# Performance work log

Hardware: AMD Instinct MI355X
Metric: run time of the kernel (lower is better)

Reference implementation:

```python
import jax, jax.numpy as jnp
import numpy as np

EMBED = 1024
HEADS = 16
HEAD_DIM = EMBED // HEADS


def setup_inputs() -> dict:
    key = jax.random.key(0)
    ks = jax.random.split(key, 8)
    b, t, d = 2, 2048, EMBED
    s = 1.0 / np.sqrt(d)
    return {
        'k': jax.random.normal(ks[0], (b, t, d), jnp.float32),
        'q': jax.random.normal(ks[1], (b, t, d), jnp.float32),
        'v': jax.random.normal(ks[2], (b, t, d), jnp.float32),
        'Wk': jax.random.normal(ks[3], (d, d), jnp.float32) * s,
        'Wq': jax.random.normal(ks[4], (d, d), jnp.float32) * s,
        'Wv': jax.random.normal(ks[5], (d, d), jnp.float32) * s,
        'Wo': jax.random.normal(ks[6], (d, d), jnp.float32) * s,
        'bo': jax.random.normal(ks[7], (d,), jnp.float32) * 0.01,
    }


def reference(k, q, v, Wk, Wq, Wv, Wo, bo):
    b, t, d = q.shape
    h, n = HEADS, HEAD_DIM
    # projections (q_prj bias=False, k/v bias=False per add_bias_kv=False)
    keys = (k @ Wk.T).reshape(b, t, h, n).transpose(0, 2, 1, 3)      # b h t n
    queries = (q @ Wq.T).reshape(b, t, h, n).transpose(0, 2, 1, 3)
    values = (v @ Wv.T).reshape(b, t, h, n).transpose(0, 2, 1, 3)
    att = jnp.einsum('bhtn,bhsn->bhts', queries, keys)               # b h t t
    att = jax.nn.softmax(att / np.sqrt(n), axis=-1)
    out = jnp.einsum('bhts,bhsn->bhtn', att, values)                 # b h t n
    out = out.transpose(0, 2, 1, 3).reshape(b, t, d)                 # b t (h n)
    return out @ Wo.T + bo
```

## Files before the change

### kernel.cpp

```cpp
#include <hip/hip_runtime.h>
#include <hip/hip_bf16.h>


typedef unsigned short u16;
typedef unsigned int   u32;
using short8 = __attribute__((ext_vector_type(8))) short;
using f32x4  = __attribute__((ext_vector_type(4))) float;

__device__ __forceinline__ u16 f2b(float f) {
    u32 u = __float_as_uint(f);
    u += 0x7FFFu + ((u >> 16) & 1u);
    return (u16)(u >> 16);
}
__device__ __forceinline__ u32 pack2(float lo, float hi) {
    union { __hip_bfloat162 h; u32 u; } c;
    c.h = __float22bfloat162_rn(make_float2(lo, hi));
    return c.u;
}
__device__ __forceinline__ float fexp2(float x) {
    return __builtin_amdgcn_exp2f(x);
}
__device__ __forceinline__ void gld_lds16(const u16* g, u16* l) {
    __builtin_amdgcn_global_load_lds(
        (const __attribute__((address_space(1))) void*)g,
        (__attribute__((address_space(3))) void*)l, 16, 0, 0);
}

__global__ __launch_bounds__(256) void convert_kernel(
    const float* s0, const float* s1, const float* s2, const float* s3,
    const float* s4, const float* s5, const float* s6,
    u16* d0, u16* d1, u16* d2, u16* d3, u16* d4, u16* d5, u16* d6)
{
    const int y = blockIdx.y;
    const float* s; u16* d; u32 n;
    switch (y) {
        case 0: s = s0; d = d0; n = 1048576; break;
        case 1: s = s1; d = d1; n = 1048576; break;
        case 2: s = s2; d = d2; n = 1048576; break;
        case 3: s = s3; d = d3; n = 262144; break;
        case 4: s = s4; d = d4; n = 262144; break;
        case 5: s = s5; d = d5; n = 262144; break;
        default: s = s6; d = d6; n = 262144; break;
    }
    for (u32 i = blockIdx.x * 256 + threadIdx.x; i < n; i += 256 * 1024) {
        float4 f = ((const float4*)s)[i];
        uint2 o; o.x = pack2(f.x, f.y); o.y = pack2(f.z, f.w);
        ((uint2*)d)[i] = o;
    }
}

template <int MODE>
__device__ __forceinline__ void gemm_core(
    const u16* __restrict__ A, const u16* __restrict__ B,
    void* __restrict__ C, const float* __restrict__ bias, float scale,
    u32 bm, u32 bn)
{
    constexpr u32 K = 1024;
    __shared__ u16 As[128 * 32];
    __shared__ u16 Bs[128 * 32];

    const int tid  = threadIdx.x;
    const int lane = tid & 63;
    const int w    = tid >> 6;
    const int wr   = w >> 1, wc = w & 1;
    const int ml   = lane & 15, g = lane >> 4;

    f32x4 acc[4][4] = {};

    const u32 srow = w * 32 + (lane >> 2);
    const u32 scol = (u32)(((lane & 3) ^ ((lane >> 3) & 3)) * 8);
    const u16* gA = A + (size_t)(bm + srow) * K + scol;
    const u16* gB = B + (size_t)(bn + srow) * K + scol;
    u16* lA = &As[w * 1024];
    u16* lB = &Bs[w * 1024];

    const u32 fsw = (u32)((g ^ ((ml >> 1) & 3)) * 8);

    for (u32 k0 = 0; k0 < K; k0 += 32) {
        __syncthreads();
        gld_lds16(gA + k0, lA);
        gld_lds16(gA + 16 * K + k0, lA + 512);
        gld_lds16(gB + k0, lB);
        gld_lds16(gB + 16 * K + k0, lB + 512);
        __syncthreads();

        short8 af[4], bf[4];
#pragma unroll
        for (int it = 0; it < 4; ++it)
            af[it] = *(const short8*)&As[(wr * 64 + it * 16 + ml) * 32 + fsw];
#pragma unroll
        for (int ct = 0; ct < 4; ++ct)
            bf[ct] = *(const short8*)&Bs[(wc * 64 + ct * 16 + ml) * 32 + fsw];
#pragma unroll
        for (int it = 0; it < 4; ++it)
#pragma unroll
            for (int ct = 0; ct < 4; ++ct)
                acc[it][ct] = __builtin_amdgcn_mfma_f32_16x16x32_bf16(
                    af[it], bf[ct], acc[it][ct], 0, 0, 0);
    }

    if (MODE == 3) {
#pragma unroll
        for (int ct = 0; ct < 4; ++ct) {
            const u32 col = bn + wc * 64 + ct * 16 + ml;
            u16* dst = (u16*)C + (col >> 11) * 2097152 + (col & 2047);
#pragma unroll
            for (int it = 0; it < 4; ++it) {
                const u32 row = bm + wr * 64 + it * 16 + g * 4;
#pragma unroll
                for (int r = 0; r < 4; ++r)
                    dst[(size_t)(row + r) * 2048] = f2b(acc[it][ct][r]);
            }
        }
    } else {
#pragma unroll
        for (int ct = 0; ct < 4; ++ct) {
            const u32 col = bn + wc * 64 + ct * 16 + ml;
            const float bv = (MODE == 2 && bias) ? bias[col] : 0.0f;
#pragma unroll
            for (int it = 0; it < 4; ++it) {
                const u32 row = bm + wr * 64 + it * 16 + g * 4;
#pragma unroll
                for (int r = 0; r < 4; ++r) {
                    const float v = acc[it][ct][r] * scale + bv;
                    if (MODE == 2) ((float*)C)[(size_t)(row + r) * 1024 + col] = v;
                    else           ((u16*)C)[(size_t)(row + r) * 1024 + col] = f2b(v);
                }
            }
        }
    }
}

__global__ __launch_bounds__(256) void proj3_kernel(
    const u16* kb, const u16* qb, const u16* vb,
    const u16* Wkb, const u16* Wqb, const u16* Wvb,
    u16* Kp, u16* Qp, u16* Vt)
{
    if (blockIdx.z == 0)
        gemm_core<0>(kb, Wkb, Kp, nullptr, 1.0f, blockIdx.y * 128, blockIdx.x * 128);
    else if (blockIdx.z == 1)
        gemm_core<0>(qb, Wqb, Qp, nullptr, 0.18033688011112042f, blockIdx.y * 128, blockIdx.x * 128);
    else
        gemm_core<3>(Wvb, vb, Vt, nullptr, 1.0f, blockIdx.x * 128, blockIdx.y * 128);
}

__global__ __launch_bounds__(256) void out_gemm_kernel(
    const u16* __restrict__ A, const u16* __restrict__ W,
    float* __restrict__ C, const float* __restrict__ bias)
{
    constexpr u32 K = 1024;
    __shared__ u16 As[64 * 32];
    __shared__ u16 Bs[128 * 32];

    const int tid  = threadIdx.x;
    const int lane = tid & 63;
    const int w    = tid >> 6;
    const int wr   = w >> 1, wc = w & 1;
    const int ml   = lane & 15, g = lane >> 4;
    const u32 bm   = blockIdx.y * 64, bn = blockIdx.x * 128;

    f32x4 acc[2][4] = {};

    const u32 scol = (u32)(((lane & 3) ^ ((lane >> 3) & 3)) * 8);
    const u16* gA = A + (size_t)(bm + w * 16 + (lane >> 2)) * K + scol;
    const u16* gB = W + (size_t)(bn + w * 32 + (lane >> 2)) * K + scol;
    u16* lA = &As[w * 512];
    u16* lB = &Bs[w * 1024];

    const u32 fsw = (u32)((g ^ ((ml >> 1) & 3)) * 8);

    for (u32 k0 = 0; k0 < K; k0 += 32) {
        __syncthreads();
        gld_lds16(gA + k0, lA);
        gld_lds16(gB + k0, lB);
        gld_lds16(gB + 16 * K + k0, lB + 512);
        __syncthreads();

        short8 af[2], bf[4];
#pragma unroll
        for (int it = 0; it < 2; ++it)
            af[it] = *(const short8*)&As[(wr * 32 + it * 16 + ml) * 32 + fsw];
#pragma unroll
        for (int ct = 0; ct < 4; ++ct)
            bf[ct] = *(const short8*)&Bs[(wc * 64 + ct * 16 + ml) * 32 + fsw];
#pragma unroll
        for (int it = 0; it < 2; ++it)
#pragma unroll
            for (int ct = 0; ct < 4; ++ct)
                acc[it][ct] = __builtin_amdgcn_mfma_f32_16x16x32_bf16(
                    af[it], bf[ct], acc[it][ct], 0, 0, 0);
    }

#pragma unroll
    for (int ct = 0; ct < 4; ++ct) {
        const u32 col = bn + wc * 64 + ct * 16 + ml;
        const float bv = bias ? bias[col] : 0.0f;
#pragma unroll
        for (int it = 0; it < 2; ++it) {
            const u32 row = bm + wr * 32 + it * 16 + g * 4;
#pragma unroll
            for (int r = 0; r < 4; ++r)
                C[(size_t)(row + r) * 1024 + col] = acc[it][ct][r] + bv;
        }
    }
}

__global__ __launch_bounds__(256, 2) void attn_kernel(
    const u16* __restrict__ Qp, const u16* __restrict__ Kp,
    const u16* __restrict__ Vt, u16* __restrict__ Op)
{
    __shared__ u16   Ps[4 * 2048];
    __shared__ float R0[4096];
    __shared__ float Lr[256];

    const int tid  = threadIdx.x;
    const int lane = tid & 63;
    const int w    = tid >> 6;
    const int ml   = lane & 15;
    const int g    = lane >> 4;
    const u32 bh   = blockIdx.y;
    const u32 b    = bh >> 4, h = bh & 15;
    const u32 t0   = blockIdx.x * 64;

    const u32 base  = b * 2048 * 1024 + h * 64;
    const u32 vbase = bh * 64 * 2048;

    short8 bq[4][2];
#pragma unroll
    for (int qt = 0; qt < 4; ++qt) {
        const u16* qr = Qp + base + (t0 + qt * 16 + ml) * 1024 + g * 8;
        bq[qt][0] = *(const short8*)qr;
        bq[qt][1] = *(const short8*)(qr + 32);
    }

    f32x4 oacc[4][4] = {};
    float l4[4] = {};

    u16* Pw = &Ps[w * 2048];
    u32* Pw32 = (u32*)Pw;

    u32 kOff = base + (w * 32 + ml) * 1024 + g * 8;
    u32 vOff = vbase + ml * 2048 + w * 32 + g * 8;

    short8 va[2][4], ka[2][2][2];
#pragma unroll
    for (int dt = 0; dt < 4; ++dt)
        va[0][dt] = *(const short8*)(Vt + vOff + dt * 32768);
#pragma unroll
    for (int sub = 0; sub < 2; ++sub) {
        const u16* kp = Kp + kOff + sub * 16384;
        ka[0][sub][0] = *(const short8*)kp;
        ka[0][sub][1] = *(const short8*)(kp + 32);
    }
    kOff += 131072; vOff += 128;

#define ATTN_STEP(CUR, NXT, PREF)                                            \
    {                                                                        \
        if (PREF) {                                                          \
            _Pragma("unroll")                                                \
            for (int dt = 0; dt < 4; ++dt)                                   \
                va[NXT][dt] = *(const short8*)(Vt + vOff + dt * 32768);      \
            _Pragma("unroll")                                                \
            for (int sub = 0; sub < 2; ++sub) {                              \
                const u16* kp = Kp + kOff + sub * 16384;                     \
                ka[NXT][sub][0] = *(const short8*)kp;                        \
                ka[NXT][sub][1] = *(const short8*)(kp + 32);                 \
            }                                                                \
            kOff += 131072; vOff += 128;                                     \
        }                                                                    \
        _Pragma("unroll")                                                    \
        for (int sub = 0; sub < 2; ++sub) {                                  \
            const u32 ch = (u32)(sub * 2 + (g >> 1));                        \
            _Pragma("unroll")                                                \
            for (int qt = 0; qt < 4; ++qt) {                                 \
                f32x4 z = {};                                                \
                z = __builtin_amdgcn_mfma_f32_16x16x32_bf16(                 \
                    ka[CUR][sub][0], bq[qt][0], z, 0, 0, 0);                 \
                z = __builtin_amdgcn_mfma_f32_16x16x32_bf16(                 \
                    ka[CUR][sub][1], bq[qt][1], z, 0, 0, 0);                 \
                const float p0 = fexp2(z[0]), p1 = fexp2(z[1]);              \
                const float p2 = fexp2(z[2]), p3 = fexp2(z[3]);              \
                l4[qt] += (p0 + p1) + (p2 + p3);                             \
                const u32 q = (u32)(qt * 16 + ml);                           \
                const u32 idx = q * 16 + ((ch ^ ((q >> 1) & 3)) << 2)        \
                                + (g & 1) * 2;                               \
                uint2 pv; pv.x = pack2(p0, p1); pv.y = pack2(p2, p3);        \
                *(uint2*)&Pw32[idx] = pv;                                    \
            }                                                                \
        }                                                                    \
        short8 pb[4];                                                        \
        _Pragma("unroll")                                                    \
        for (int qt = 0; qt < 4; ++qt) {                                     \
            const u32 q = (u32)(qt * 16 + ml);                               \
            pb[qt] = *(const short8*)&Pw[q * 32 + ((g ^ ((q >> 1) & 3)) * 8)]; \
        }                                                                    \
        _Pragma("unroll")                                                    \
        for (int dt = 0; dt < 4; ++dt)                                       \
            _Pragma("unroll")                                                \
            for (int qt = 0; qt < 4; ++qt)                                   \
                oacc[dt][qt] = __builtin_amdgcn_mfma_f32_16x16x32_bf16(      \
                    va[CUR][dt], pb[qt], oacc[dt][qt], 0, 0, 0);             \
    }

    for (int it = 0; it < 7; ++it) {
        ATTN_STEP(0, 1, true)
        ATTN_STEP(1, 0, true)
    }
    ATTN_STEP(0, 1, true)
    ATTN_STEP(1, 0, false)
#undef ATTN_STEP

#pragma unroll
    for (int qt = 0; qt < 4; ++qt) {
        l4[qt] += __shfl_xor(l4[qt], 16);
        l4[qt] += __shfl_xor(l4[qt], 32);
    }
    if (g == 0) {
#pragma unroll
        for (int qt = 0; qt < 4; ++qt) Lr[w * 64 + qt * 16 + ml] = l4[qt];
    }
    __syncthreads();
    float* R1 = (float*)Ps;

#define WRITE_R(Rp)                                                          \
    {_Pragma("unroll") for (int dt = 0; dt < 4; ++dt)                        \
     _Pragma("unroll") for (int qt = 0; qt < 4; ++qt)                        \
     _Pragma("unroll") for (int r = 0; r < 4; ++r)                           \
        (Rp)[(dt * 16 + g * 4 + r) * 64 + qt * 16 + ml] = oacc[dt][qt][r];}
#define ADD_R(Rp)                                                            \
    {_Pragma("unroll") for (int dt = 0; dt < 4; ++dt)                        \
     _Pragma("unroll") for (int qt = 0; qt < 4; ++qt)                        \
     _Pragma("unroll") for (int r = 0; r < 4; ++r)                           \
        oacc[dt][qt][r] += (Rp)[(dt * 16 + g * 4 + r) * 64 + qt * 16 + ml];}

    if (w == 1) WRITE_R(R0)
    if (w == 3) WRITE_R(R1)
    __syncthreads();
    if (w == 0) ADD_R(R0)
    if (w == 2) ADD_R(R1)
    __syncthreads();
    if (w == 2) WRITE_R(R0)
    __syncthreads();
    if (w == 0) {
        ADD_R(R0)
#pragma unroll
        for (int qt = 0; qt < 4; ++qt) {
            const u32 q = (u32)(qt * 16 + ml);
            const float inv = 1.0f / (Lr[q] + Lr[64 + q] + Lr[128 + q] + Lr[192 + q]);
            const u32 row = (b * 2048 + t0 + q) * 1024 + h * 64;
#pragma unroll
            for (int dt = 0; dt < 4; ++dt) {
                const u32 ci = row + dt * 16 + g * 4;
                *(u32*)&Op[ci]     = pack2(oacc[dt][qt][0] * inv, oacc[dt][qt][1] * inv);
                *(u32*)&Op[ci + 2] = pack2(oacc[dt][qt][2] * inv, oacc[dt][qt][3] * inv);
            }
        }
    }
#undef WRITE_R
#undef ADD_R
}

extern "C" void kernel_launch(void* const* d_in, const int* in_sizes, int n_in,
                              void* d_out, int out_size, void* d_ws, size_t ws_size,
                              hipStream_t stream)
{
    const float* kin = (const float*)d_in[0];
    const float* qin = (const float*)d_in[1];
    const float* vin = (const float*)d_in[2];
    const float* Wk  = (const float*)d_in[3];
    const float* Wq  = (const float*)d_in[4];
    const float* Wv  = (const float*)d_in[5];
    const float* Wo  = (const float*)d_in[6];
    const float* bo  = (const float*)d_in[7];
    float* out = (float*)d_out;

    const size_t ACT = 4194304;
    const size_t WSZ = 1048576;

    u16* kb  = (u16*)d_ws;
    u16* qb  = kb + ACT;
    u16* vb  = qb + ACT;
    u16* Wkb = vb + ACT;
    u16* Wqb = Wkb + WSZ;
    u16* Wvb = Wqb + WSZ;
    u16* Wob = Wvb + WSZ;
    u16* Kp  = Wob + WSZ;
    u16* Qp  = Kp + ACT;
    u16* Vt  = Qp + ACT;
    u16* Op  = kb;

    convert_kernel<<<dim3(1024, 7), 256, 0, stream>>>(
        kin, qin, vin, Wk, Wq, Wv, Wo, kb, qb, vb, Wkb, Wqb, Wvb, Wob);
    proj3_kernel<<<dim3(8, 32, 3), 256, 0, stream>>>(
        kb, qb, vb, Wkb, Wqb, Wvb, Kp, Qp, Vt);
    attn_kernel<<<dim3(32, 32), 256, 0, stream>>>(Qp, Kp, Vt, Op);
    out_gemm_kernel<<<dim3(8, 64), 256, 0, stream>>>(Op, Wob, out, bo);
}
```

Before: 233.6 us.

## Split attention work by query rows per wave instead of splitting keys

Each wave now owns 16 query rows and walks all 2048 keys, where before every wave covered all 64 queries over a quarter of the keys. This removes the cross-wave LDS reduction of output accumulators and row sums along with its barriers, shrinks shared memory, and raises the launch-bounds occupancy target from 2 to 4. In exchange, each K/V tile loaded per wave now feeds only one query tile instead of four, so K/V global/L2 traffic rises about fourfold and the loop runs four times as many serial steps with less MFMA work between loads.

```diff
diff --git a/kernel.cpp b/kernel.cpp
--- a/kernel.cpp
+++ b/kernel.cpp
@@ -205,13 +205,11 @@
     }
 }
 
-__global__ __launch_bounds__(256, 2) void attn_kernel(
+__global__ __launch_bounds__(256, 4) void attn_kernel(
     const u16* __restrict__ Qp, const u16* __restrict__ Kp,
     const u16* __restrict__ Vt, u16* __restrict__ Op)
 {
-    __shared__ u16   Ps[4 * 2048];
-    __shared__ float R0[4096];
-    __shared__ float Lr[256];
+    __shared__ u16 Ps[4 * 512];
 
     const int tid  = threadIdx.x;
     const int lane = tid & 63;
@@ -225,22 +223,21 @@
     const u32 base  = b * 2048 * 1024 + h * 64;
     const u32 vbase = bh * 64 * 2048;
 
-    short8 bq[4][2];
-#pragma unroll
-    for (int qt = 0; qt < 4; ++qt) {
-        const u16* qr = Qp + base + (t0 + qt * 16 + ml) * 1024 + g * 8;
-        bq[qt][0] = *(const short8*)qr;
-        bq[qt][1] = *(const short8*)(qr + 32);
-    }
-
-    f32x4 oacc[4][4] = {};
-    float l4[4] = {};
-
-    u16* Pw = &Ps[w * 2048];
+    short8 bq[2];
+    {
+        const u16* qr = Qp + base + (t0 + w * 16 + ml) * 1024 + g * 8;
+        bq[0] = *(const short8*)qr;
+        bq[1] = *(const short8*)(qr + 32);
+    }
+
+    f32x4 oacc[4] = {};
+    float l4 = 0.0f;
+
+    u16* Pw = &Ps[w * 512];
     u32* Pw32 = (u32*)Pw;
 
-    u32 kOff = base + (w * 32 + ml) * 1024 + g * 8;
-    u32 vOff = vbase + ml * 2048 + w * 32 + g * 8;
+    u32 kOff = base + ml * 1024 + g * 8;
+    u32 vOff = vbase + ml * 2048 + g * 8;
 
     short8 va[2][4], ka[2][2][2];
 #pragma unroll
@@ -252,7 +249,7 @@
         ka[0][sub][0] = *(const short8*)kp;
         ka[0][sub][1] = *(const short8*)(kp + 32);
     }
-    kOff += 131072; vOff += 128;
+    kOff += 32768; vOff += 32;
 
 #define ATTN_STEP(CUR, NXT, PREF)                                            \
     {                                                                        \
@@ -266,43 +263,37 @@
                 ka[NXT][sub][0] = *(const short8*)kp;                        \
                 ka[NXT][sub][1] = *(const short8*)(kp + 32);                 \
             }                                                                \
-            kOff += 131072; vOff += 128;                                     \
+            kOff += 32768; vOff += 32;                                       \
         }                                                                    \
         _Pragma("unroll")                                                    \
         for (int sub = 0; sub < 2; ++sub) {                                  \
             const u32 ch = (u32)(sub * 2 + (g >> 1));                        \
-            _Pragma("unroll")                                                \
-            for (int qt = 0; qt < 4; ++qt) {                                 \
-                f32x4 z = {};                                                \
-                z = __builtin_amdgcn_mfma_f32_16x16x32_bf16(                 \
-                    ka[CUR][sub][0], bq[qt][0], z, 0, 0, 0);                 \
-                z = __builtin_amdgcn_mfma_f32_16x16x32_bf16(                 \
-                    ka[CUR][sub][1], bq[qt][1], z, 0, 0, 0);                 \
-                const float p0 = fexp2(z[0]), p1 = fexp2(z[1]);              \
-                const float p2 = fexp2(z[2]), p3 = fexp2(z[3]);              \
-                l4[qt] += (p0 + p1) + (p2 + p3);                             \
-                const u32 q = (u32)(qt * 16 + ml);                           \
-                const u32 idx = q * 16 + ((ch ^ ((q >> 1) & 3)) << 2)        \
-                                + (g & 1) * 2;                               \
-                uint2 pv; pv.x = pack2(p0, p1); pv.y = pack2(p2, p3);        \
-                *(uint2*)&Pw32[idx] = pv;                                    \
-            }                                                                \
+            f32x4 z = {};                                                    \
+            z = __builtin_amdgcn_mfma_f32_16x16x32_bf16(                     \
+                ka[CUR][sub][0], bq[0], z, 0, 0, 0);                         \
+            z = __builtin_amdgcn_mfma_f32_16x16x32_bf16(                     \
+                ka[CUR][sub][1], bq[1], z, 0, 0, 0);                         \
+            const float p0 = fexp2(z[0]), p1 = fexp2(z[1]);                  \
+            const float p2 = fexp2(z[2]), p3 = fexp2(z[3]);                  \
+            l4 += (p0 + p1) + (p2 + p3);                                     \
+            const u32 q = (u32)ml;                                           \
+            const u32 idx = q * 16 + ((ch ^ ((q >> 1) & 3)) << 2)            \
+                            + (g & 1) * 2;                                   \
+            uint2 pv; pv.x = pack2(p0, p1); pv.y = pack2(p2, p3);            \
+            *(uint2*)&Pw32[idx] = pv;                                        \
         }                                                                    \
-        short8 pb[4];                                                        \
-        _Pragma("unroll")                                                    \
-        for (int qt = 0; qt < 4; ++qt) {                                     \
-            const u32 q = (u32)(qt * 16 + ml);                               \
-            pb[qt] = *(const short8*)&Pw[q * 32 + ((g ^ ((q >> 1) & 3)) * 8)]; \
+        short8 pb;                                                           \
+        {                                                                    \
+            const u32 q = (u32)ml;                                           \
+            pb = *(const short8*)&Pw[q * 32 + ((g ^ ((q >> 1) & 3)) * 8)];   \
         }                                                                    \
         _Pragma("unroll")                                                    \
         for (int dt = 0; dt < 4; ++dt)                                       \
-            _Pragma("unroll")                                                \
-            for (int qt = 0; qt < 4; ++qt)                                   \
-                oacc[dt][qt] = __builtin_amdgcn_mfma_f32_16x16x32_bf16(      \
-                    va[CUR][dt], pb[qt], oacc[dt][qt], 0, 0, 0);             \
-    }
-
-    for (int it = 0; it < 7; ++it) {
+            oacc[dt] = __builtin_amdgcn_mfma_f32_16x16x32_bf16(              \
+                va[CUR][dt], pb, oacc[dt], 0, 0, 0);                         \
+    }
+
+    for (int it = 0; it < 31; ++it) {
         ATTN_STEP(0, 1, true)
         ATTN_STEP(1, 0, true)
     }
@@ -310,54 +301,20 @@
     ATTN_STEP(1, 0, false)
 #undef ATTN_STEP
 
-#pragma unroll
-    for (int qt = 0; qt < 4; ++qt) {
-        l4[qt] += __shfl_xor(l4[qt], 16);
-        l4[qt] += __shfl_xor(l4[qt], 32);
-    }
-    if (g == 0) {
-#pragma unroll
-        for (int qt = 0; qt < 4; ++qt) Lr[w * 64 + qt * 16 + ml] = l4[qt];
-    }
-    __syncthreads();
-    float* R1 = (float*)Ps;
-
-#define WRITE_R(Rp)                                                          \
-    {_Pragma("unroll") for (int dt = 0; dt < 4; ++dt)                        \
-     _Pragma("unroll") for (int qt = 0; qt < 4; ++qt)                        \
-     _Pragma("unroll") for (int r = 0; r < 4; ++r)                           \
-        (Rp)[(dt * 16 + g * 4 + r) * 64 + qt * 16 + ml] = oacc[dt][qt][r];}
-#define ADD_R(Rp)                                                            \
-    {_Pragma("unroll") for (int dt = 0; dt < 4; ++dt)                        \
-     _Pragma("unroll") for (int qt = 0; qt < 4; ++qt)                        \
-     _Pragma("unroll") for (int r = 0; r < 4; ++r)                           \
-        oacc[dt][qt][r] += (Rp)[(dt * 16 + g * 4 + r) * 64 + qt * 16 + ml];}
-
-    if (w == 1) WRITE_R(R0)
-    if (w == 3) WRITE_R(R1)
-    __syncthreads();
-    if (w == 0) ADD_R(R0)
-    if (w == 2) ADD_R(R1)
-    __syncthreads();
-    if (w == 2) WRITE_R(R0)
-    __syncthreads();
-    if (w == 0) {
-        ADD_R(R0)
-#pragma unroll
-        for (int qt = 0; qt < 4; ++qt) {
-            const u32 q = (u32)(qt * 16 + ml);
-            const float inv = 1.0f / (Lr[q] + Lr[64 + q] + Lr[128 + q] + Lr[192 + q]);
-            const u32 row = (b * 2048 + t0 + q) * 1024 + h * 64;
-#pragma unroll
-            for (int dt = 0; dt < 4; ++dt) {
-                const u32 ci = row + dt * 16 + g * 4;
-                *(u32*)&Op[ci]     = pack2(oacc[dt][qt][0] * inv, oacc[dt][qt][1] * inv);
-                *(u32*)&Op[ci + 2] = pack2(oacc[dt][qt][2] * inv, oacc[dt][qt][3] * inv);
-            }
+    l4 += __shfl_xor(l4, 16);
+    l4 += __shfl_xor(l4, 32);
+    const float inv = 1.0f / l4;
+
+    {
+        const u32 q = (u32)(w * 16 + ml);
+        const u32 row = (b * 2048 + t0 + q) * 1024 + h * 64;
+#pragma unroll
+        for (int dt = 0; dt < 4; ++dt) {
+            const u32 ci = row + dt * 16 + g * 4;
+            *(u32*)&Op[ci]     = pack2(oacc[dt][0] * inv, oacc[dt][1] * inv);
+            *(u32*)&Op[ci + 2] = pack2(oacc[dt][2] * inv, oacc[dt][3] * inv);
         }
     }
-#undef WRITE_R
-#undef ADD_R
 }
 
 extern "C" void kernel_launch(void* const* d_in, const int* in_sizes, int n_in,
```

After: 390.0 us. 1.67x slower.

## Split attention block into query-pair x key-half warps, shrink LDS and reduction

Applied to the files above, without the earlier changes.

Reorganizes the attention kernel so the four warps form two query groups of 32 rows, each split across two key halves, instead of all four warps sharing 64 queries and splitting keys four ways. Per-warp accumulator and P-buffer state halves, the cross-warp reduction drops from a three-stage tree to a single exchange, and launch bounds rise to allow three blocks per CU. The cost is each warp walking twice as many key/value tiles, so K/V are loaded twice per block for the same total work, and register pressure under the tighter bound may force spills.

```diff
diff --git a/kernel.cpp b/kernel.cpp
--- a/kernel.cpp
+++ b/kernel.cpp
@@ -205,17 +205,19 @@
     }
 }
 
-__global__ __launch_bounds__(256, 2) void attn_kernel(
+__global__ __launch_bounds__(256, 3) void attn_kernel(
     const u16* __restrict__ Qp, const u16* __restrict__ Kp,
     const u16* __restrict__ Vt, u16* __restrict__ Op)
 {
-    __shared__ u16   Ps[4 * 2048];
-    __shared__ float R0[4096];
-    __shared__ float Lr[256];
+    __shared__ u16   Ps[4 * 1024];
+    __shared__ float Rs[2][2048];
+    __shared__ float Ls[2][32];
 
     const int tid  = threadIdx.x;
     const int lane = tid & 63;
     const int w    = tid >> 6;
+    const int wq   = w >> 1;
+    const int ws   = w & 1;
     const int ml   = lane & 15;
     const int g    = lane >> 4;
     const u32 bh   = blockIdx.y;
@@ -225,22 +227,22 @@
     const u32 base  = b * 2048 * 1024 + h * 64;
     const u32 vbase = bh * 64 * 2048;
 
-    short8 bq[4][2];
-#pragma unroll
-    for (int qt = 0; qt < 4; ++qt) {
-        const u16* qr = Qp + base + (t0 + qt * 16 + ml) * 1024 + g * 8;
+    short8 bq[2][2];
+#pragma unroll
+    for (int qt = 0; qt < 2; ++qt) {
+        const u16* qr = Qp + base + (t0 + wq * 32 + qt * 16 + ml) * 1024 + g * 8;
         bq[qt][0] = *(const short8*)qr;
         bq[qt][1] = *(const short8*)(qr + 32);
     }
 
-    f32x4 oacc[4][4] = {};
-    float l4[4] = {};
-
-    u16* Pw = &Ps[w * 2048];
+    f32x4 oacc[4][2] = {};
+    float l4[2] = {};
+
+    u16* Pw = &Ps[w * 1024];
     u32* Pw32 = (u32*)Pw;
 
-    u32 kOff = base + (w * 32 + ml) * 1024 + g * 8;
-    u32 vOff = vbase + ml * 2048 + w * 32 + g * 8;
+    u32 kOff = base + (ws * 32 + ml) * 1024 + g * 8;
+    u32 vOff = vbase + ml * 2048 + ws * 32 + g * 8;
 
     short8 va[2][4], ka[2][2][2];
 #pragma unroll
@@ -252,7 +254,7 @@
         ka[0][sub][0] = *(const short8*)kp;
         ka[0][sub][1] = *(const short8*)(kp + 32);
     }
-    kOff += 131072; vOff += 128;
+    kOff += 65536; vOff += 64;
 
 #define ATTN_STEP(CUR, NXT, PREF)                                            \
     {                                                                        \
@@ -266,13 +268,13 @@
                 ka[NXT][sub][0] = *(const short8*)kp;                        \
                 ka[NXT][sub][1] = *(const short8*)(kp + 32);                 \
             }                                                                \
-            kOff += 131072; vOff += 128;                                     \
+            kOff += 65536; vOff += 64;                                       \
         }                                                                    \
         _Pragma("unroll")                                                    \
         for (int sub = 0; sub < 2; ++sub) {                                  \
             const u32 ch = (u32)(sub * 2 + (g >> 1));                        \
             _Pragma("unroll")                                                \
-            for (int qt = 0; qt < 4; ++qt) {                                 \
+            for (int qt = 0; qt < 2; ++qt) {                                 \
                 f32x4 z = {};                                                \
                 z = __builtin_amdgcn_mfma_f32_16x16x32_bf16(                 \
                     ka[CUR][sub][0], bq[qt][0], z, 0, 0, 0);                 \
@@ -288,21 +290,21 @@
                 *(uint2*)&Pw32[idx] = pv;                                    \
             }                                                                \
         }                                                                    \
-        short8 pb[4];                                                        \
+        short8 pb[2];                                                        \
         _Pragma("unroll")                                                    \
-        for (int qt = 0; qt < 4; ++qt) {                                     \
+        for (int qt = 0; qt < 2; ++qt) {                                     \
             const u32 q = (u32)(qt * 16 + ml);                               \
             pb[qt] = *(const short8*)&Pw[q * 32 + ((g ^ ((q >> 1) & 3)) * 8)]; \
         }                                                                    \
         _Pragma("unroll")                                                    \
         for (int dt = 0; dt < 4; ++dt)                                       \
             _Pragma("unroll")                                                \
-            for (int qt = 0; qt < 4; ++qt)                                   \
+            for (int qt = 0; qt < 2; ++qt)                                   \
                 oacc[dt][qt] = __builtin_amdgcn_mfma_f32_16x16x32_bf16(      \
                     va[CUR][dt], pb[qt], oacc[dt][qt], 0, 0, 0);             \
     }
 
-    for (int it = 0; it < 7; ++it) {
+    for (int it = 0; it < 15; ++it) {
         ATTN_STEP(0, 1, true)
         ATTN_STEP(1, 0, true)
     }
@@ -311,42 +313,37 @@
 #undef ATTN_STEP
 
 #pragma unroll
-    for (int qt = 0; qt < 4; ++qt) {
+    for (int qt = 0; qt < 2; ++qt) {
         l4[qt] += __shfl_xor(l4[qt], 16);
         l4[qt] += __shfl_xor(l4[qt], 32);
     }
-    if (g == 0) {
-#pragma unroll
-        for (int qt = 0; qt < 4; ++qt) Lr[w * 64 + qt * 16 + ml] = l4[qt];
+
+    if (ws == 1) {
+#pragma unroll
+        for (int dt = 0; dt < 4; ++dt)
+#pragma unroll
+            for (int qt = 0; qt < 2; ++qt)
+#pragma unroll
+                for (int r = 0; r < 4; ++r)
+                    Rs[wq][(dt * 16 + g * 4 + r) * 32 + qt * 16 + ml] = oacc[dt][qt][r];
+        if (g == 0) {
+#pragma unroll
+            for (int qt = 0; qt < 2; ++qt) Ls[wq][qt * 16 + ml] = l4[qt];
+        }
     }
     __syncthreads();
-    float* R1 = (float*)Ps;
-
-#define WRITE_R(Rp)                                                          \
-    {_Pragma("unroll") for (int dt = 0; dt < 4; ++dt)                        \
-     _Pragma("unroll") for (int qt = 0; qt < 4; ++qt)                        \
-     _Pragma("unroll") for (int r = 0; r < 4; ++r)                           \
-        (Rp)[(dt * 16 + g * 4 + r) * 64 + qt * 16 + ml] = oacc[dt][qt][r];}
-#define ADD_R(Rp)                                                            \
-    {_Pragma("unroll") for (int dt = 0; dt < 4; ++dt)                        \
-     _Pragma("unroll") for (int qt = 0; qt < 4; ++qt)                        \
-     _Pragma("unroll") for (int r = 0; r < 4; ++r)                           \
-        oacc[dt][qt][r] += (Rp)[(dt * 16 + g * 4 + r) * 64 + qt * 16 + ml];}
-
-    if (w == 1) WRITE_R(R0)
-    if (w == 3) WRITE_R(R1)
-    __syncthreads();
-    if (w == 0) ADD_R(R0)
-    if (w == 2) ADD_R(R1)
-    __syncthreads();
-    if (w == 2) WRITE_R(R0)
-    __syncthreads();
-    if (w == 0) {
-        ADD_R(R0)
-#pragma unroll
-        for (int qt = 0; qt < 4; ++qt) {
-            const u32 q = (u32)(qt * 16 + ml);
-            const float inv = 1.0f / (Lr[q] + Lr[64 + q] + Lr[128 + q] + Lr[192 + q]);
+    if (ws == 0) {
+#pragma unroll
+        for (int dt = 0; dt < 4; ++dt)
+#pragma unroll
+            for (int qt = 0; qt < 2; ++qt)
+#pragma unroll
+                for (int r = 0; r < 4; ++r)
+                    oacc[dt][qt][r] += Rs[wq][(dt * 16 + g * 4 + r) * 32 + qt * 16 + ml];
+#pragma unroll
+        for (int qt = 0; qt < 2; ++qt) {
+            const u32 q = (u32)(wq * 32 + qt * 16 + ml);
+            const float inv = 1.0f / (l4[qt] + Ls[wq][qt * 16 + ml]);
             const u32 row = (b * 2048 + t0 + q) * 1024 + h * 64;
 #pragma unroll
             for (int dt = 0; dt < 4; ++dt) {
@@ -356,8 +353,6 @@
             }
         }
     }
-#undef WRITE_R
-#undef ADD_R
 }
 
 extern "C" void kernel_launch(void* const* d_in, const int* in_sizes, int n_in,
```

After: 281.8 us. +20.6%, slower.
